# Performance work log

Measured on AMD Instinct MI355X. Metric: run time of the kernel, lower is better.

Reference implementation:

```python
import jax, jax.numpy as jnp
import numpy as np

BETA = 0.25
K = 4096


def setup_inputs() -> dict:
    key = jax.random.key(0)
    k1, k2 = jax.random.split(key)
    z = jax.random.normal(k1, (32, 256, 32, 32), dtype=jnp.float32)
    # matches torch init: uniform(-1/k, 1/k)
    embedding = jax.random.uniform(k2, (K, 256), dtype=jnp.float32,
                                   minval=-1.0 / K, maxval=1.0 / K)
    return {"z": z, "embedding": embedding}


def reference(z, embedding):
    b, d, h, w = z.shape
    k = embedding.shape[0]
    # (b d h w) -> (n d)
    z_flat = jnp.transpose(z, (0, 2, 3, 1)).reshape(-1, d)
    # squared euclidean distances, (n, k)
    distances = (jnp.sum(z_flat * z_flat, axis=-1, keepdims=True)
                 + jnp.sum(embedding * embedding, axis=-1)
                 - 2.0 * jnp.einsum('nd,kd->nk', z_flat, embedding))
    encoding_indices = jnp.argmin(distances, axis=1)
    encodings_onehot = jax.nn.one_hot(encoding_indices, k, dtype=z.dtype)
    zq_flat = embedding[encoding_indices]
    z_quantized = jnp.transpose(zq_flat.reshape(b, h, w, d), (0, 3, 1, 2))
    loss_encoder = jnp.mean((jax.lax.stop_gradient(z_quantized) - z) ** 2)
    loss_codebook = jnp.mean((z_quantized - jax.lax.stop_gradient(z)) ** 2)
    loss = BETA * loss_encoder + loss_codebook
    # straight-through estimator
    z_quantized_st = z + jax.lax.stop_gradient(z_quantized - z)
    # perplexity of codebook usage
    enc_mean = jnp.mean(encodings_onehot, axis=0)
    perplexity = jnp.exp(-jnp.sum(enc_mean * jnp.log(enc_mean + 1e-10)))
    return (z_quantized_st, loss, perplexity, encodings_onehot,
            encoding_indices, distances)
```

## Files before the change

### kernel.cpp

```cpp
#include <hip/hip_runtime.h>
#include <hip/hip_bf16.h>

typedef unsigned short u16;
typedef unsigned int u32;
typedef unsigned long long u64;
typedef __attribute__((ext_vector_type(8))) short bf16x8;
typedef __attribute__((ext_vector_type(4))) float f32x4;

#define NROWS 32768
#define KCODES 4096
#define DDIM 256
#define HW 1024
#define ZSTRIDE_B 262144ULL

#define OFF_ZQ   0ULL
#define OFF_LOSS 8388608ULL
#define OFF_PERP 8388609ULL
#define OFF_OH   8388610ULL
#define OFF_IDX  142606338ULL
#define OFF_DIST 142639106ULL

#define T_ZH 16777280ULL
#define T_EH 25165888ULL

#define WS_IDX    0
#define WS_COUNTS 131072
#define WS_EN2    147456
#define WS_ZN2    163840
#define WS_PART   294912
#define WS_BDIST  295424
#define WS_BMIN   524288

__global__ __launch_bounds__(64) void k_prep_e_en2(const float* __restrict__ emb,
                                                   float* __restrict__ en2,
                                                   u16* __restrict__ Ehh,
                                                   unsigned* __restrict__ counts) {
    int k = blockIdx.x;
    int l = threadIdx.x;
    float4 v = *(const float4*)(emb + (size_t)k * DDIM + l * 4);
    float s = v.x * v.x + v.y * v.y + v.z * v.z + v.w * v.w;
    #pragma unroll
    for (int m = 32; m; m >>= 1) s += __shfl_xor(s, m);
    if (l == 0) { en2[k] = s; counts[k] = 0u; }
    float vv[4] = {v.x, v.y, v.z, v.w};
    u16 ho[4];
    #pragma unroll
    for (int j = 0; j < 4; ++j) {
        __hip_bfloat16 hb = __float2bfloat16(vv[j]);
        ho[j] = *(u16*)&hb;
    }
    *(ushort4*)(Ehh + (size_t)k * DDIM + l * 4) = make_ushort4(ho[0], ho[1], ho[2], ho[3]);
}

__global__ __launch_bounds__(256) void k_zn2(const float* __restrict__ z,
                                             float* __restrict__ zn2) {
    int n = blockIdx.x * 256 + threadIdx.x;
    int b = n >> 10, hw = n & 1023;
    const float* zp = z + (size_t)b * ZSTRIDE_B + hw;
    float s = 0.f;
    #pragma unroll 8
    for (int d = 0; d < DDIM; ++d) {
        float v = zp[(size_t)d * HW];
        s = fmaf(v, v, s);
    }
    zn2[n] = s;
}

__global__ __launch_bounds__(256) void k_prep_z(const float* __restrict__ z,
                                                u16* __restrict__ Zhh) {
    __shared__ float t[32][132];
    const int tid = threadIdx.x;
    const int h0 = blockIdx.x * 128, d0 = blockIdx.y * 32, b = blockIdx.z;
    const float* zp = z + (size_t)b * ZSTRIDE_B;
    {
        int hq = (tid & 31) << 2;
        int dr = tid >> 5;
        #pragma unroll
        for (int p = 0; p < 4; ++p) {
            int d = p * 8 + dr;
            float4 v = *(const float4*)(zp + (size_t)(d0 + d) * HW + h0 + hq);
            *(float4*)&t[d][hq] = v;
        }
    }
    __syncthreads();
    {
        int nr = tid >> 1;
        int half = tid & 1;
        int n = b * HW + h0 + nr;
        u16 hv[16];
        #pragma unroll
        for (int i = 0; i < 16; ++i) {
            float v = t[half * 16 + i][nr];
            __hip_bfloat16 hb = __float2bfloat16(v);
            hv[i] = *(u16*)&hb;
        }
        u16* dst = Zhh + (size_t)n * DDIM + d0 + half * 16;
        #pragma unroll
        for (int q = 0; q < 4; ++q)
            *(ushort4*)(dst + q * 4) = *(ushort4*)&hv[q * 4];
    }
}

__global__ __launch_bounds__(256) void k_dist_mfma(
    const u16* __restrict__ Zhh, const u16* __restrict__ Ehh,
    const float* __restrict__ zn2, const float* __restrict__ en2,
    float* __restrict__ dist, float* __restrict__ bmin)
{
    __shared__ __align__(16) u16 smem[16384];
    u16* As = smem;
    u16* Bs = smem + 8192;
    float* Ct = (float*)smem;

    const int tid = threadIdx.x;
    const int w = tid >> 6, l = tid & 63;
    const int n0 = blockIdx.x * 128, k0 = blockIdx.y * 128;
    const int kb = blockIdx.y;
    const int wr = w >> 1, wc = w & 1;

    int goff[4], loff[4];
    #pragma unroll
    for (int it = 0; it < 4; ++it) {
        int o = (it << 12) + (w << 10) + (l << 4);
        int r = o >> 7;
        int c16 = (o >> 4) & 7;
        int gs = c16 ^ (r & 7);
        goff[it] = r * DDIM + gs * 8;
        loff[it] = (it << 11) + (w << 9);
    }

    f32x4 acc[4][4];
    #pragma unroll
    for (int m = 0; m < 4; ++m)
        #pragma unroll
        for (int n = 0; n < 4; ++n)
            acc[m][n] = (f32x4){0.f, 0.f, 0.f, 0.f};

    const int lr = l & 15, ks = l >> 4;
    const int ra = wr * 64 + lr, rb = wc * 64 + lr;

    const u16* Ap = Zhh + (size_t)n0 * DDIM;
    const u16* Bp = Ehh + (size_t)k0 * DDIM;
    for (int st = 0; st < 4; ++st) {
        const int d0 = st * 64;
        #pragma unroll
        for (int it = 0; it < 4; ++it) {
            __builtin_amdgcn_global_load_lds(
                (const __attribute__((address_space(1))) void*)(Ap + d0 + goff[it]),
                (__attribute__((address_space(3))) void*)(As + loff[it]), 16, 0, 0);
            __builtin_amdgcn_global_load_lds(
                (const __attribute__((address_space(1))) void*)(Bp + d0 + goff[it]),
                (__attribute__((address_space(3))) void*)(Bs + loff[it]), 16, 0, 0);
        }
        __syncthreads();
        #pragma unroll
        for (int kk = 0; kk < 2; ++kk) {
            bf16x8 af[4], bfr[4];
            #pragma unroll
            for (int m = 0; m < 4; ++m) {
                int rr = ra + m * 16;
                af[m] = *(const bf16x8*)&As[rr * 64 + ((kk * 4 + ks) ^ (rr & 7)) * 8];
            }
            #pragma unroll
            for (int n = 0; n < 4; ++n) {
                int rr = rb + n * 16;
                bfr[n] = *(const bf16x8*)&Bs[rr * 64 + ((kk * 4 + ks) ^ (rr & 7)) * 8];
            }
            #pragma unroll
            for (int m = 0; m < 4; ++m)
                #pragma unroll
                for (int n = 0; n < 4; ++n)
                    acc[m][n] = __builtin_amdgcn_mfma_f32_16x16x32_bf16(
                        af[m], bfr[n], acc[m][n], 0, 0, 0);
        }
        __syncthreads();
    }

    float ev[4];
    #pragma unroll
    for (int n = 0; n < 4; ++n) ev[n] = en2[k0 + wc * 64 + n * 16 + lr];

    #pragma unroll
    for (int m = 0; m < 4; ++m) {
        #pragma unroll
        for (int r = 0; r < 4; ++r) {
            int row = n0 + wr * 64 + m * 16 + ks * 4 + r;
            float t = zn2[row];
            int ridx = wr * 16 + ks * 4 + r;
            float rm = 3.4e38f;
            #pragma unroll
            for (int n = 0; n < 4; ++n) {
                float s  = __fadd_rn(t, ev[n]);
                float m2 = __fmul_rn(2.0f, acc[m][n][r]);
                float dv = __fsub_rn(s, m2);
                Ct[ridx * 132 + wc * 64 + n * 16 + lr] = dv;
                rm = fminf(rm, dv);
            }
            #pragma unroll
            for (int msk = 1; msk < 16; msk <<= 1)
                rm = fminf(rm, __shfl_xor(rm, msk));
            if (lr == 0)
                bmin[((size_t)row * 32 + kb) * 2 + wc] = rm;
        }
        __syncthreads();
        #pragma unroll
        for (int rr = 0; rr < 8; ++rr) {
            int rid = w * 8 + rr;
            int grow = n0 + m * 16 + (rid >> 4) * 64 + (rid & 15);
            float a = Ct[rid * 132 + l * 2];
            float b = Ct[rid * 132 + l * 2 + 1];
            *(float2*)(dist + (size_t)grow * KCODES + k0 + l * 2) = make_float2(a, b);
        }
        __syncthreads();
    }
}

__global__ __launch_bounds__(256) void k_select(
    const float* __restrict__ dist, const float* __restrict__ z,
    const float* __restrict__ emb, const float* __restrict__ zn2,
    const float* __restrict__ en2, const float* __restrict__ bmin,
    u32* __restrict__ idxarr, float* __restrict__ bdist)
{
    const int l = threadIdx.x & 63;
    const int row = blockIdx.x * 4 + (threadIdx.x >> 6);
    float bm = bmin[(size_t)row * 64 + l];
    float mn = bm;
    #pragma unroll
    for (int m = 1; m < 64; m <<= 1) mn = fminf(mn, __shfl_xor(mn, m));
    const float thr = mn + 1e-3f;
    u64 qual = __ballot(bm <= thr);

    const int b = row >> 10, hw = row & 1023;
    const float* zp = z + (size_t)b * ZSTRIDE_B + hw;
    float z0 = zp[(size_t)(l * 4 + 0) * HW];
    float z1 = zp[(size_t)(l * 4 + 1) * HW];
    float z2 = zp[(size_t)(l * 4 + 2) * HW];
    float z3 = zp[(size_t)(l * 4 + 3) * HW];
    const float zr = zn2[row];

    u64 best = ~0ull;
    int prev_kb = -1;
    u64 qq = qual;
    while (qq) {
        int bit = __ffsll(qq) - 1; qq &= qq - 1;
        int kb = bit >> 1;
        if (kb == prev_kb) continue;
        prev_kb = kb;
        const float* dr = dist + (size_t)row * KCODES + kb * 128;
        float2 d2 = *(const float2*)(dr + l * 2);
        u64 c0 = __ballot(d2.x <= thr);
        u64 c1 = __ballot(d2.y <= thr);
        u64 any = c0 | c1;
        while (any) {
            int src = __ffsll(any) - 1; any &= any - 1;
            #pragma unroll
            for (int e = 0; e < 2; ++e) {
                u64 msk = e ? c1 : c0;
                if (!((msk >> src) & 1)) continue;
                int k = kb * 128 + src * 2 + e;
                float4 e4 = *(const float4*)(emb + (size_t)k * DDIM + l * 4);
                float p = 0.f;
                p = fmaf(z0, e4.x, p);
                p = fmaf(z1, e4.y, p);
                p = fmaf(z2, e4.z, p);
                p = fmaf(z3, e4.w, p);
                #pragma unroll
                for (int m = 1; m < 64; m <<= 1) p += __shfl_xor(p, m);
                float dh = __fsub_rn(__fadd_rn(zr, en2[k]), __fmul_rn(2.0f, p));
                u32 ub = __float_as_uint(dh);
                ub = (ub & 0x80000000u) ? ~ub : (ub | 0x80000000u);
                u64 cand = ((u64)ub << 32) | (u32)k;
                best = cand < best ? cand : best;
            }
        }
    }
    if (l == 0) {
        idxarr[row] = (u32)(best & 0xffffffffu);
        u32 ub = (u32)(best >> 32);
        u32 fb = (ub & 0x80000000u) ? (ub & 0x7fffffffu) : ~ub;
        bdist[row] = __uint_as_float(fb);
    }
}

__global__ __launch_bounds__(256) void k_zq_oh(const float* __restrict__ emb,
                                               const u32* __restrict__ idxarr,
                                               const float* __restrict__ bdist,
                                               unsigned* __restrict__ counts,
                                               float* __restrict__ out,
                                               float* __restrict__ partials) {
    const int bid = blockIdx.x;
    if (bid < 8192) {
        const int l = threadIdx.x & 63;
        const int n = bid * 4 + (threadIdx.x >> 6);
        const int idx = (int)idxarr[n];
        float* base = out + OFF_OH + (size_t)n * KCODES;
        #pragma unroll
        for (int i = 0; i < 16; ++i) {
            int c0 = i * 256 + l * 4;
            float2 a, b2;
            a.x  = (idx == c0)     ? 1.0f : 0.0f;
            a.y  = (idx == c0 + 1) ? 1.0f : 0.0f;
            b2.x = (idx == c0 + 2) ? 1.0f : 0.0f;
            b2.y = (idx == c0 + 3) ? 1.0f : 0.0f;
            *(float2*)(base + c0) = a;
            *(float2*)(base + c0 + 2) = b2;
        }
    } else {
        const int bz = bid - 8192;
        int n = bz * 256 + threadIdx.x;
        unsigned idx = idxarr[n];
        out[OFF_IDX + n] = (float)idx;
        atomicAdd(counts + idx, 1u);
        int b = n >> 10, hw = n & 1023;
        const float* ep = emb + (size_t)idx * DDIM;
        float* oq = out + OFF_ZQ + (size_t)b * ZSTRIDE_B + hw;
        #pragma unroll 2
        for (int d = 0; d < DDIM; d += 4) {
            float4 e4 = *(const float4*)(ep + d);
            oq[(size_t)(d + 0) * HW] = e4.x;
            oq[(size_t)(d + 1) * HW] = e4.y;
            oq[(size_t)(d + 2) * HW] = e4.z;
            oq[(size_t)(d + 3) * HW] = e4.w;
        }
        __shared__ float red[256];
        red[threadIdx.x] = bdist[n];
        __syncthreads();
        for (int st = 128; st > 0; st >>= 1) {
            if (threadIdx.x < st) red[threadIdx.x] += red[threadIdx.x + st];
            __syncthreads();
        }
        if (threadIdx.x == 0) partials[bz] = red[0];
    }
}

__global__ __launch_bounds__(256) void k_final(const unsigned* __restrict__ counts,
                                               const float* __restrict__ partials,
                                               float* __restrict__ out) {
    __shared__ float red[256];
    int t = threadIdx.x;
    red[t] = (t < 128) ? partials[t] : 0.f;
    __syncthreads();
    for (int st = 128; st > 0; st >>= 1) {
        if (t < st) red[t] += red[t + st];
        __syncthreads();
    }
    float loss = 1.25f * (red[0] / 8388608.0f);
    __syncthreads();
    float h = 0.f;
    for (int k = t; k < KCODES; k += 256) {
        float p = (float)counts[k] * (1.0f / 32768.0f);
        h -= p * logf(p + 1e-10f);
    }
    red[t] = h;
    __syncthreads();
    for (int st = 128; st > 0; st >>= 1) {
        if (t < st) red[t] += red[t + st];
        __syncthreads();
    }
    if (t == 0) {
        out[OFF_LOSS] = loss;
        out[OFF_PERP] = expf(red[0]);
    }
}

extern "C" void kernel_launch(void* const* d_in, const int* in_sizes, int n_in,
                              void* d_out, int out_size, void* d_ws, size_t ws_size,
                              hipStream_t stream) {
    (void)in_sizes; (void)n_in; (void)out_size; (void)ws_size;
    const float* z = (const float*)d_in[0];
    const float* emb = (const float*)d_in[1];
    float* out = (float*)d_out;
    char* ws = (char*)d_ws;
    u32* idxarr = (u32*)(ws + WS_IDX);
    unsigned* counts = (unsigned*)(ws + WS_COUNTS);
    float* en2 = (float*)(ws + WS_EN2);
    float* zn2 = (float*)(ws + WS_ZN2);
    float* partials = (float*)(ws + WS_PART);
    float* bdist = (float*)(ws + WS_BDIST);
    float* bmin = (float*)(ws + WS_BMIN);

    u16* Zhh = (u16*)(out + T_ZH);
    u16* Ehh = (u16*)(out + T_EH);
    float* dist = out + OFF_DIST;

    k_prep_z<<<dim3(8, 8, 32), 256, 0, stream>>>(z, Zhh);
    k_prep_e_en2<<<KCODES, 64, 0, stream>>>(emb, en2, Ehh, counts);
    k_zn2<<<NROWS / 256, 256, 0, stream>>>(z, zn2);
    k_dist_mfma<<<dim3(NROWS / 128, KCODES / 128), 256, 0, stream>>>(
        Zhh, Ehh, zn2, en2, dist, bmin);
    k_select<<<NROWS / 4, 256, 0, stream>>>(dist, z, emb, zn2, en2, bmin,
                                            idxarr, bdist);
    k_zq_oh<<<8320, 256, 0, stream>>>(emb, idxarr, bdist, counts, out, partials);
    k_final<<<1, 256, 0, stream>>>(counts, partials, out);
}
```

Baseline: 558.2 us.

## Double-buffer LDS staging of Z/E tiles in distance MFMA kernel

Splits the 256-wide reduction into eight 32-wide stages held in two LDS buffers, so the global-to-LDS loads for the next stage are issued before the MFMAs on the current one run. Manual vmcnt waits and raw s_barrier replace __syncthreads, and the swizzle pattern is changed to fit the 32-column tile. The zn2 and en2 norms are now loaded before the main loop and pinned in registers so their latency overlaps the GEMM. In exchange there are twice as many barriers per K-depth, the hand-written waitcnt ordering is fragile, and register pressure goes up.

After: 555.8 us. About the same (-0.4%).

```diff
diff --git a/kernel.cpp b/kernel.cpp
--- a/kernel.cpp
+++ b/kernel.cpp
@@ -116,17 +116,52 @@
     const int n0 = blockIdx.x * 128, k0 = blockIdx.y * 128;
     const int kb = blockIdx.y;
     const int wr = w >> 1, wc = w & 1;
-
-    int goff[4], loff[4];
-    #pragma unroll
-    for (int it = 0; it < 4; ++it) {
-        int o = (it << 12) + (w << 10) + (l << 4);
-        int r = o >> 7;
-        int c16 = (o >> 4) & 7;
-        int gs = c16 ^ (r & 7);
+    const int lr = l & 15, ks = l >> 4;
+    const int ra = wr * 64 + lr, rb = wc * 64 + lr;
+
+    int goff[2], loff[2];
+    #pragma unroll
+    for (int it = 0; it < 2; ++it) {
+        int o = (w << 10) + (it << 12) + (l << 4);
+        int r = o >> 6;
+        int c16 = (o >> 4) & 3;
+        int gs = c16 ^ ((r >> 1) & 3);
         goff[it] = r * DDIM + gs * 8;
-        loff[it] = (it << 11) + (w << 9);
-    }
+        loff[it] = (w << 9) + (it << 11);
+    }
+
+    float zrow[16], ev[4];
+    #pragma unroll
+    for (int m = 0; m < 4; ++m)
+        #pragma unroll
+        for (int r = 0; r < 4; ++r)
+            zrow[m * 4 + r] = zn2[n0 + wr * 64 + m * 16 + ks * 4 + r];
+    #pragma unroll
+    for (int n = 0; n < 4; ++n) ev[n] = en2[k0 + wc * 64 + n * 16 + lr];
+    asm volatile("" : "+v"(zrow[0]), "+v"(zrow[1]), "+v"(zrow[2]), "+v"(zrow[3]),
+                      "+v"(zrow[4]), "+v"(zrow[5]), "+v"(zrow[6]), "+v"(zrow[7]),
+                      "+v"(zrow[8]), "+v"(zrow[9]), "+v"(zrow[10]), "+v"(zrow[11]),
+                      "+v"(zrow[12]), "+v"(zrow[13]), "+v"(zrow[14]), "+v"(zrow[15]),
+                      "+v"(ev[0]), "+v"(ev[1]), "+v"(ev[2]), "+v"(ev[3]));
+    __builtin_amdgcn_sched_barrier(0);
+
+    const u16* Ap = Zhh + (size_t)n0 * DDIM;
+    const u16* Bp = Ehh + (size_t)k0 * DDIM;
+
+    auto STAGE = [&](int buf, int st) {
+        const int d0 = st * 32;
+        #pragma unroll
+        for (int it = 0; it < 2; ++it) {
+            __builtin_amdgcn_global_load_lds(
+                (const __attribute__((address_space(1))) void*)(Ap + d0 + goff[it]),
+                (__attribute__((address_space(3))) void*)(As + buf * 4096 + loff[it]),
+                16, 0, 0);
+            __builtin_amdgcn_global_load_lds(
+                (const __attribute__((address_space(1))) void*)(Bp + d0 + goff[it]),
+                (__attribute__((address_space(3))) void*)(Bs + buf * 4096 + loff[it]),
+                16, 0, 0);
+        }
+    };
 
     f32x4 acc[4][4];
     #pragma unroll
@@ -135,56 +170,51 @@
         for (int n = 0; n < 4; ++n)
             acc[m][n] = (f32x4){0.f, 0.f, 0.f, 0.f};
 
-    const int lr = l & 15, ks = l >> 4;
-    const int ra = wr * 64 + lr, rb = wc * 64 + lr;
-
-    const u16* Ap = Zhh + (size_t)n0 * DDIM;
-    const u16* Bp = Ehh + (size_t)k0 * DDIM;
-    for (int st = 0; st < 4; ++st) {
-        const int d0 = st * 64;
-        #pragma unroll
-        for (int it = 0; it < 4; ++it) {
-            __builtin_amdgcn_global_load_lds(
-                (const __attribute__((address_space(1))) void*)(Ap + d0 + goff[it]),
-                (__attribute__((address_space(3))) void*)(As + loff[it]), 16, 0, 0);
-            __builtin_amdgcn_global_load_lds(
-                (const __attribute__((address_space(1))) void*)(Bp + d0 + goff[it]),
-                (__attribute__((address_space(3))) void*)(Bs + loff[it]), 16, 0, 0);
-        }
-        __syncthreads();
-        #pragma unroll
-        for (int kk = 0; kk < 2; ++kk) {
-            bf16x8 af[4], bfr[4];
+    STAGE(0, 0);
+    int cur = 0;
+    #pragma unroll
+    for (int st = 0; st < 8; ++st) {
+        if (st < 7) {
+            STAGE(cur ^ 1, st + 1);
+            asm volatile("s_waitcnt vmcnt(4)" ::: "memory");
+        } else {
+            asm volatile("s_waitcnt vmcnt(0)" ::: "memory");
+        }
+        __builtin_amdgcn_sched_barrier(0);
+        asm volatile("s_barrier" ::: "memory");
+
+        const u16* Ac = As + cur * 4096;
+        const u16* Bc = Bs + cur * 4096;
+        bf16x8 af[4], bfr[4];
+        #pragma unroll
+        for (int m = 0; m < 4; ++m) {
+            int rr = ra + m * 16;
+            af[m] = *(const bf16x8*)&Ac[rr * 32 + (ks ^ ((rr >> 1) & 3)) * 8];
+        }
+        #pragma unroll
+        for (int n = 0; n < 4; ++n) {
+            int rr = rb + n * 16;
+            bfr[n] = *(const bf16x8*)&Bc[rr * 32 + (ks ^ ((rr >> 1) & 3)) * 8];
+        }
+        #pragma unroll
+        for (int m = 0; m < 4; ++m)
             #pragma unroll
-            for (int m = 0; m < 4; ++m) {
-                int rr = ra + m * 16;
-                af[m] = *(const bf16x8*)&As[rr * 64 + ((kk * 4 + ks) ^ (rr & 7)) * 8];
-            }
-            #pragma unroll
-            for (int n = 0; n < 4; ++n) {
-                int rr = rb + n * 16;
-                bfr[n] = *(const bf16x8*)&Bs[rr * 64 + ((kk * 4 + ks) ^ (rr & 7)) * 8];
-            }
-            #pragma unroll
-            for (int m = 0; m < 4; ++m)
-                #pragma unroll
-                for (int n = 0; n < 4; ++n)
-                    acc[m][n] = __builtin_amdgcn_mfma_f32_16x16x32_bf16(
-                        af[m], bfr[n], acc[m][n], 0, 0, 0);
-        }
-        __syncthreads();
-    }
-
-    float ev[4];
-    #pragma unroll
-    for (int n = 0; n < 4; ++n) ev[n] = en2[k0 + wc * 64 + n * 16 + lr];
+            for (int n = 0; n < 4; ++n)
+                acc[m][n] = __builtin_amdgcn_mfma_f32_16x16x32_bf16(
+                    af[m], bfr[n], acc[m][n], 0, 0, 0);
+
+        asm volatile("s_waitcnt lgkmcnt(0)" ::: "memory");
+        __builtin_amdgcn_sched_barrier(0);
+        asm volatile("s_barrier" ::: "memory");
+        cur ^= 1;
+    }
 
     #pragma unroll
     for (int m = 0; m < 4; ++m) {
         #pragma unroll
         for (int r = 0; r < 4; ++r) {
             int row = n0 + wr * 64 + m * 16 + ks * 4 + r;
-            float t = zn2[row];
+            float t = zrow[m * 4 + r];
             int ridx = wr * 16 + ks * 4 + r;
             float rm = 3.4e38f;
             #pragma unroll
```
